# Kernel tuning notes

Measured on AMD Instinct MI355X. Metric: run time of the kernel, lower is better.

Reference implementation:

```python
import jax, jax.numpy as jnp
import numpy as np

EMBED = 1024
HEADS = 16
HEAD_DIM = EMBED // HEADS


def _rope(t):
    # t: (B, S, H, D) -> rotary embedding applied over last dim (GPT-NeoX rotate-half)
    B, S, H, D = t.shape
    half = D // 2
    inv_freq = 1.0 / (10000.0 ** (jnp.arange(0, half, dtype=jnp.float32) / half))
    freqs = jnp.arange(S, dtype=jnp.float32)[:, None] * inv_freq[None, :]  # (S, half)
    cos = jnp.cos(freqs)[None, :, None, :]
    sin = jnp.sin(freqs)[None, :, None, :]
    t1, t2 = t[..., :half], t[..., half:]
    return jnp.concatenate([t1 * cos - t2 * sin, t2 * cos + t1 * sin], axis=-1)


def setup_inputs() -> dict:
    key = jax.random.key(0)
    k1, k2, k3 = jax.random.split(key, 3)
    B, S = 2, 2048
    x = jax.random.normal(k1, (B, S, EMBED), dtype=jnp.float32)
    attn_mask = jnp.ones((B, S), dtype=bool)
    w_qkv = jax.random.normal(k2, (EMBED, 3 * EMBED), dtype=jnp.float32) * (1.0 / np.sqrt(EMBED))
    w_out = jax.random.normal(k3, (EMBED, EMBED), dtype=jnp.float32) * (1.0 / np.sqrt(EMBED))
    return {"x": x, "attn_mask": attn_mask, "w_qkv": w_qkv, "w_out": w_out, "is_causal": 1}


def reference(x, attn_mask, w_qkv, w_out, is_causal):
    B, S, E = x.shape
    qkv = x @ w_qkv                                   # (B, S, 3E)
    q, k, v = jnp.split(qkv, 3, axis=-1)
    q = q.reshape(B, S, HEADS, HEAD_DIM)
    k = k.reshape(B, S, HEADS, HEAD_DIM)
    v = v.reshape(B, S, HEADS, HEAD_DIM)
    q = _rope(q)
    k = _rope(k)
    scale = 1.0 / np.sqrt(HEAD_DIM)
    scores = jnp.einsum('bqhd,bkhd->bhqk', q, k) * scale  # (B, H, S, S)
    neg = jnp.asarray(-1e30, dtype=scores.dtype)
    if is_causal:
        causal = jnp.tril(jnp.ones((S, S), dtype=bool))
        scores = jnp.where(causal[None, None], scores, neg)
    else:
        scores = jnp.where(attn_mask[:, None, None, :], scores, neg)
    attn = jax.nn.softmax(scores, axis=-1)
    y = jnp.einsum('bhqk,bkhd->bqhd', attn, v).reshape(B, S, E)
    return y @ w_out
```

## Files before the change

kernel.cpp:

```cpp
#include <hip/hip_runtime.h>
#include <hip/hip_bf16.h>
#include <stdint.h>

typedef float v4f __attribute__((ext_vector_type(4)));
typedef short v8s __attribute__((ext_vector_type(8)));

#define LOG2E 1.44269504088896f
#define QSCALE (0.125f * LOG2E)
#define SOFTMAX_OFF 16.0f

__device__ __forceinline__ unsigned short f2bf(float f) {
    unsigned int u = __float_as_uint(f);
    u += 0x7fffu + ((u >> 16) & 1u);
    return (unsigned short)(u >> 16);
}

#define LDS_FENCE() __builtin_amdgcn_fence(__ATOMIC_ACQ_REL, "workgroup")

__device__ __forceinline__ void gload_lds16(const unsigned short* g, unsigned short* s) {
    __builtin_amdgcn_global_load_lds(
        (const __attribute__((address_space(1))) unsigned int*)g,
        (__attribute__((address_space(3))) unsigned int*)s, 16, 0, 0);
}

__global__ void k_prep(const float* __restrict__ x,
                       const float* __restrict__ w_qkv,
                       const float* __restrict__ w_out,
                       unsigned short* __restrict__ xb,
                       unsigned short* __restrict__ wqkvT,
                       unsigned short* __restrict__ woutT,
                       float2* __restrict__ rope) {
    __shared__ unsigned short tile[64][65];
    int id = blockIdx.x, t = threadIdx.x;
    if (id < 1024) {
        int base = id * 256 + t;
#pragma unroll
        for (int k = 0; k < 4; ++k) {
            int i = base + k * 262144;
            float4 v = ((const float4*)x)[i];
            ushort4 o;
            o.x = f2bf(v.x); o.y = f2bf(v.y); o.z = f2bf(v.z); o.w = f2bf(v.w);
            ((ushort4*)xb)[i] = o;
        }
        return;
    }
    id -= 1024;
    if (id < 256) {
        int idx = id * 256 + t;
        int s = idx >> 5, d = idx & 31;
        float inv = __expf(-(float)d * 0.28782313662425572f);
        float sn, cs;
        sincosf((float)s * inv, &sn, &cs);
        rope[idx] = make_float2(cs, sn);
        return;
    }
    id -= 256;
    const float* src; unsigned short* dst; int N, kb, nb;
    if (id < 768) { src = w_qkv; dst = wqkvT; N = 3072; nb = (id % 48) * 64; kb = (id / 48) * 64; }
    else { id -= 768; src = w_out; dst = woutT; N = 1024; nb = (id % 16) * 64; kb = (id / 16) * 64; }
    const int K = 1024;
    for (int i = 0; i < 16; ++i) {
        int e = t + i * 256;
        int n_l = e & 63, k_l = e >> 6;
        tile[n_l][k_l] = f2bf(src[(size_t)(kb + k_l) * N + nb + n_l]);
    }
    __syncthreads();
    for (int i = 0; i < 16; ++i) {
        int e = t + i * 256;
        int k_l = e & 63, n_l = e >> 6;
        dst[(size_t)(nb + n_l) * K + kb + k_l] = tile[n_l][k_l];
    }
}

__global__ __launch_bounds__(256) void k_gemm_qkv(
    const unsigned short* __restrict__ A,
    const unsigned short* __restrict__ Bt,
    const float2* __restrict__ rope,
    unsigned short* __restrict__ Qg,
    unsigned short* __restrict__ Kg,
    unsigned short* __restrict__ Vt) {
    const int K = 1024;
    __shared__ __align__(16) union {
        struct { unsigned short Ab[2][4096], Bb[2][4096]; } g;
        unsigned short vt[2][64][136];
    } sm;
    const int t = threadIdx.x;
    const int w = t >> 6, l = t & 63, quad = l >> 4, ln = l & 15;
    const int wm = (w >> 1) * 64, wn = (w & 1) * 64;
    const int mb = blockIdx.y * 128, nb = blockIdx.x * 128;

    v4f acc[4][4];
#pragma unroll
    for (int i = 0; i < 4; ++i)
#pragma unroll
        for (int j = 0; j < 4; ++j) acc[i][j] = (v4f){0.f, 0.f, 0.f, 0.f};

    auto stage = [&](int buf, int k0) {
#pragma unroll
        for (int u = 0; u < 2; ++u) {
            int e = t + u * 256;
            gload_lds16(A + (size_t)(mb + (e >> 2)) * K + k0 + (e & 3) * 8,
                        &sm.g.Ab[buf][(w * 64 + u * 256) * 8]);
            gload_lds16(Bt + (size_t)(nb + (e >> 2)) * K + k0 + (e & 3) * 8,
                        &sm.g.Bb[buf][(w * 64 + u * 256) * 8]);
        }
    };

    stage(0, 0);
    int buf = 0;
    for (int itk = 0; itk < 32; ++itk) {
        __syncthreads();
        if (itk + 1 < 32) stage(buf ^ 1, (itk + 1) * 32);
        v8s af[4], bfr[4];
#pragma unroll
        for (int i = 0; i < 4; ++i)
            af[i] = *(const v8s*)&sm.g.Ab[buf][(wm + i * 16 + ln) * 32 + quad * 8];
#pragma unroll
        for (int j = 0; j < 4; ++j)
            bfr[j] = *(const v8s*)&sm.g.Bb[buf][(wn + j * 16 + ln) * 32 + quad * 8];
#pragma unroll
        for (int i = 0; i < 4; ++i)
#pragma unroll
            for (int j = 0; j < 4; ++j)
                acc[i][j] = __builtin_amdgcn_mfma_f32_16x16x32_bf16(
                    af[i], bfr[j], acc[i][j], 0, 0, 0);
        buf ^= 1;
    }

    if (nb >= 2048) {
        __syncthreads();
        const int hh = wn >> 6;
#pragma unroll
        for (int i = 0; i < 4; ++i)
#pragma unroll
            for (int j = 0; j < 4; ++j) {
                int d = j * 16 + ln;
#pragma unroll
                for (int r = 0; r < 4; ++r)
                    sm.vt[hh][d][wm + i * 16 + quad * 4 + r] = f2bf(acc[i][j][r]);
            }
        __syncthreads();
        const int hbase = (nb & 1023) >> 6;
        const int b = mb >> 11, sbase = mb & 2047;
#pragma unroll
        for (int i = 0; i < 8; ++i) {
            int c = t + i * 256;
            int h2 = c >> 10, dd = (c >> 4) & 63, off = (c & 15) * 8;
            v8s val = *(const v8s*)&sm.vt[h2][dd][off];
            *(v8s*)(Vt + ((size_t)((b * 16 + hbase + h2) * 64 + dd) * 2048 + sbase + off)) = val;
        }
        return;
    }

    const int region = (nb + wn) >> 10;
    const int h = ((nb + wn) & 1023) >> 6;
    unsigned short* dst = region == 0 ? Qg : Kg;
    const float scale = region == 0 ? QSCALE : 1.0f;
#pragma unroll
    for (int jj = 0; jj < 2; ++jj) {
        const float2* rp = rope + jj * 16 + ln;
#pragma unroll
        for (int i = 0; i < 4; ++i)
#pragma unroll
            for (int r = 0; r < 4; ++r) {
                int row = mb + wm + i * 16 + quad * 4 + r;
                int s = row & 2047, b = row >> 11;
                float2 cs = rp[s * 32];
                float t1 = acc[i][jj][r], t2 = acc[i][jj + 2][r];
                size_t base = ((size_t)(b * 16 + h) * 2048 + s) * 64;
                dst[base + jj * 16 + ln]      = f2bf((t1 * cs.x - t2 * cs.y) * scale);
                dst[base + jj * 16 + ln + 32] = f2bf((t2 * cs.x + t1 * cs.y) * scale);
            }
    }
}

__global__ __launch_bounds__(256) void k_gemm_out(
    const unsigned short* __restrict__ A,
    const unsigned short* __restrict__ Bt,
    float* __restrict__ C) {
    const int K = 1024, N = 1024;
    __shared__ __align__(16) unsigned short Ab[2][4096];
    __shared__ __align__(16) unsigned short Bb[2][4096];
    const int t = threadIdx.x;
    const int w = t >> 6, l = t & 63, quad = l >> 4, ln = l & 15;
    const int wm = (w >> 1) * 64, wn = (w & 1) * 64;
    const int mb = blockIdx.y * 128, nb = blockIdx.x * 128;

    v4f acc[4][4];
#pragma unroll
    for (int i = 0; i < 4; ++i)
#pragma unroll
        for (int j = 0; j < 4; ++j) acc[i][j] = (v4f){0.f, 0.f, 0.f, 0.f};

    auto stage = [&](int buf, int k0) {
#pragma unroll
        for (int u = 0; u < 2; ++u) {
            int e = t + u * 256;
            gload_lds16(A + (size_t)(mb + (e >> 2)) * K + k0 + (e & 3) * 8,
                        &Ab[buf][(w * 64 + u * 256) * 8]);
            gload_lds16(Bt + (size_t)(nb + (e >> 2)) * K + k0 + (e & 3) * 8,
                        &Bb[buf][(w * 64 + u * 256) * 8]);
        }
    };

    stage(0, 0);
    int buf = 0;
    for (int itk = 0; itk < 32; ++itk) {
        __syncthreads();
        if (itk + 1 < 32) stage(buf ^ 1, (itk + 1) * 32);
        v8s af[4], bfr[4];
#pragma unroll
        for (int i = 0; i < 4; ++i)
            af[i] = *(const v8s*)&Ab[buf][(wm + i * 16 + ln) * 32 + quad * 8];
#pragma unroll
        for (int j = 0; j < 4; ++j)
            bfr[j] = *(const v8s*)&Bb[buf][(wn + j * 16 + ln) * 32 + quad * 8];
#pragma unroll
        for (int i = 0; i < 4; ++i)
#pragma unroll
            for (int j = 0; j < 4; ++j)
                acc[i][j] = __builtin_amdgcn_mfma_f32_16x16x32_bf16(
                    af[i], bfr[j], acc[i][j], 0, 0, 0);
        buf ^= 1;
    }

#pragma unroll
    for (int i = 0; i < 4; ++i) {
        int r0 = mb + wm + i * 16 + quad * 4;
#pragma unroll
        for (int j = 0; j < 4; ++j) {
            int c0 = nb + wn + j * 16 + ln;
#pragma unroll
            for (int r = 0; r < 4; ++r)
                C[(size_t)(r0 + r) * N + c0] = acc[i][j][r];
        }
    }
}

__global__ __launch_bounds__(256) void k_flash(
    const unsigned short* __restrict__ Qg,
    const unsigned short* __restrict__ Kg,
    const unsigned short* __restrict__ Vt,
    unsigned short* __restrict__ Og) {
    __shared__ __align__(16) unsigned short Kb[2][64 * 64];
    __shared__ __align__(16) unsigned short Vb[2][64 * 64];
    __shared__ __align__(16) unsigned short P[4][16][72];

    const int id = blockIdx.x;
    const int xcd = id & 7, slot = id >> 3;
    const int bh = xcd * 4 + (slot & 3);
    const int qt = 31 - (slot >> 2);
    const int qbase = qt * 64;
    const int nit = qt + 1;

    const int t = threadIdx.x, w = t >> 6, l = t & 63, quad = l >> 4, ln = l & 15;
    const int b = bh >> 4, h = bh & 15;

    const unsigned short* Qp = Qg + (size_t)bh * 2048 * 64;
    const unsigned short* Kp = Kg + (size_t)bh * 2048 * 64;
    const unsigned short* Vp = Vt + (size_t)bh * 64 * 2048;

    unsigned kst[2], vst[2];
    int cchunk = l & 7, rloc = l >> 3;
#pragma unroll
    for (int j = 0; j < 2; ++j) {
        int c = w + j * 4;
        int rr = c * 8 + rloc;
        int g = (cchunk + rr) & 7;
        kst[j] = (unsigned)(rr * 64 + g * 8);
        vst[j] = (unsigned)(rr * 2048 + g * 8);
    }
    const int c0 = ((quad - ln) & 7) * 8;
    const int c1 = ((quad + 4 - ln) & 7) * 8;
    const v8s ones = {0x3F80, 0x3F80, 0x3F80, 0x3F80, 0x3F80, 0x3F80, 0x3F80, 0x3F80};

    const int qrow = qbase + w * 16 + ln;
    v8s qf0 = *(const v8s*)(Qp + (size_t)qrow * 64 + quad * 8);
    v8s qf1 = *(const v8s*)(Qp + (size_t)qrow * 64 + quad * 8 + 32);

    v4f oacc[5];
#pragma unroll
    for (int dt = 0; dt < 5; ++dt) oacc[dt] = (v4f){0.f, 0.f, 0.f, 0.f};

    auto stage = [&](int buf, int kvb) {
        const unsigned short* kg = Kp + (size_t)kvb * 64;
        const unsigned short* vg = Vp + kvb;
#pragma unroll
        for (int j = 0; j < 2; ++j) {
            int c = w + j * 4;
            gload_lds16(kg + kst[j], &Kb[buf][c * 512]);
            gload_lds16(vg + vst[j], &Vb[buf][c * 512]);
        }
    };

    auto compute = [&](int buf, int it) {
        v4f sc[4];
#pragma unroll
        for (int kt = 0; kt < 4; ++kt) {
            int row = kt * 16 + ln;
            v8s k0 = *(const v8s*)&Kb[buf][row * 64 + c0];
            v8s k1 = *(const v8s*)&Kb[buf][row * 64 + c1];
            sc[kt] = (v4f){0.f, 0.f, 0.f, 0.f};
            sc[kt] = __builtin_amdgcn_mfma_f32_16x16x32_bf16(qf0, k0, sc[kt], 0, 0, 0);
            sc[kt] = __builtin_amdgcn_mfma_f32_16x16x32_bf16(qf1, k1, sc[kt], 0, 0, 0);
        }
        if (it == qt) {
            int q0 = qbase + w * 16 + quad * 4;
#pragma unroll
            for (int kt = 0; kt < 4; ++kt) {
                int kv = qbase + kt * 16 + ln;
#pragma unroll
                for (int r = 0; r < 4; ++r)
                    if (kv > q0 + r) sc[kt][r] = -1e30f;
            }
        }
#pragma unroll
        for (int kt = 0; kt < 4; ++kt)
#pragma unroll
            for (int r = 0; r < 4; ++r)
                sc[kt][r] = exp2f(sc[kt][r] - SOFTMAX_OFF);

#pragma unroll
        for (int kt = 0; kt < 4; ++kt) {
            union { __hip_bfloat162 hh; unsigned int u; } p01, p23;
            p01.hh = __float22bfloat162_rn(make_float2(sc[kt][0], sc[kt][1]));
            p23.hh = __float22bfloat162_rn(make_float2(sc[kt][2], sc[kt][3]));
            P[w][quad * 4 + 0][kt * 16 + ln] = (unsigned short)p01.u;
            P[w][quad * 4 + 1][kt * 16 + ln] = (unsigned short)(p01.u >> 16);
            P[w][quad * 4 + 2][kt * 16 + ln] = (unsigned short)p23.u;
            P[w][quad * 4 + 3][kt * 16 + ln] = (unsigned short)(p23.u >> 16);
        }
        LDS_FENCE();
        v8s pf0 = *(const v8s*)&P[w][ln][quad * 8];
        v8s pf1 = *(const v8s*)&P[w][ln][quad * 8 + 32];
        LDS_FENCE();
#pragma unroll
        for (int dt = 0; dt < 4; ++dt) {
            int row = dt * 16 + ln;
            v8s v0 = *(const v8s*)&Vb[buf][row * 64 + c0];
            v8s v1 = *(const v8s*)&Vb[buf][row * 64 + c1];
            oacc[dt] = __builtin_amdgcn_mfma_f32_16x16x32_bf16(pf0, v0, oacc[dt], 0, 0, 0);
            oacc[dt] = __builtin_amdgcn_mfma_f32_16x16x32_bf16(pf1, v1, oacc[dt], 0, 0, 0);
        }
        oacc[4] = __builtin_amdgcn_mfma_f32_16x16x32_bf16(pf0, ones, oacc[4], 0, 0, 0);
        oacc[4] = __builtin_amdgcn_mfma_f32_16x16x32_bf16(pf1, ones, oacc[4], 0, 0, 0);
    };

    stage(0, 0);
    int it = 0;
    for (;;) {
        __syncthreads();
        stage(1, (it + 1) * 64);
        compute(0, it);
        if (++it >= nit) break;
        __syncthreads();
        stage(0, (it + 1) * 64);
        compute(1, it);
        if (++it >= nit) break;
    }

    float rden[4];
#pragma unroll
    for (int r = 0; r < 4; ++r) rden[r] = 1.f / oacc[4][r];
#pragma unroll
    for (int dt = 0; dt < 4; ++dt)
#pragma unroll
        for (int r = 0; r < 4; ++r) {
            int s = qbase + w * 16 + quad * 4 + r;
            Og[(size_t)(b * 2048 + s) * 1024 + h * 64 + dt * 16 + ln] =
                f2bf(oacc[dt][r] * rden[r]);
        }
}

extern "C" void kernel_launch(void* const* d_in, const int* in_sizes, int n_in,
                              void* d_out, int out_size, void* d_ws, size_t ws_size,
                              hipStream_t stream) {
    const float* x     = (const float*)d_in[0];
    const float* w_qkv = (const float*)d_in[2];
    const float* w_out = (const float*)d_in[3];
    char* ws = (char*)d_ws;

    unsigned short* xb    = (unsigned short*)(ws);
    unsigned short* wqkvT = (unsigned short*)(ws + (size_t)(8 << 20));
    unsigned short* woutT = (unsigned short*)(ws + (size_t)(14 << 20));
    unsigned short* Qg    = (unsigned short*)(ws + (size_t)(16 << 20));
    unsigned short* Kg    = (unsigned short*)(ws + (size_t)(24 << 20));
    unsigned short* Vt    = (unsigned short*)(ws + (size_t)(32 << 20));
    unsigned short* Og    = (unsigned short*)(ws + (size_t)(40 << 20));
    float2*         rope  = (float2*)(ws + (size_t)(48 << 20));

    k_prep<<<2304, 256, 0, stream>>>(x, w_qkv, w_out, xb, wqkvT, woutT, rope);
    k_gemm_qkv<<<dim3(24, 32), 256, 0, stream>>>(xb, wqkvT, rope, Qg, Kg, Vt);
    k_flash<<<1024, 256, 0, stream>>>(Qg, Kg, Vt, Og);
    k_gemm_out<<<dim3(8, 32), 256, 0, stream>>>(Og, woutT, (float*)d_out);
}
```

Baseline: 195.2 us.

## Triple-buffer GEMM K-loop with partial vmcnt waits instead of full syncthreads

Both GEMM kernels move from double to triple LDS buffering and prefetch two K-tiles ahead. The barrier now waits only until the oldest stage's four global-to-LDS loads have landed (vmcnt(4)) rather than draining every outstanding load, so one tile stays in flight during compute. This is meant to hide global load latency behind the MFMA work, at the cost of 50% more LDS per block, which may lower occupancy. It also depends on the compiler's vmcnt accounting matching the inline waitcnt.

```diff
diff --git a/kernel.cpp b/kernel.cpp
--- a/kernel.cpp
+++ b/kernel.cpp
@@ -22,6 +22,19 @@
         (const __attribute__((address_space(1))) unsigned int*)g,
         (__attribute__((address_space(3))) unsigned int*)s, 16, 0, 0);
 }
+
+#define PIPE_BARRIER_KEEP4()                                   \
+    do {                                                       \
+        asm volatile("s_waitcnt vmcnt(4)" ::: "memory");       \
+        __builtin_amdgcn_s_barrier();                          \
+        asm volatile("" ::: "memory");                         \
+    } while (0)
+#define PIPE_BARRIER_DRAIN()                                   \
+    do {                                                       \
+        asm volatile("s_waitcnt vmcnt(0)" ::: "memory");       \
+        __builtin_amdgcn_s_barrier();                          \
+        asm volatile("" ::: "memory");                         \
+    } while (0)
 
 __global__ void k_prep(const float* __restrict__ x,
                        const float* __restrict__ w_qkv,
@@ -81,7 +94,7 @@
     unsigned short* __restrict__ Vt) {
     const int K = 1024;
     __shared__ __align__(16) union {
-        struct { unsigned short Ab[2][4096], Bb[2][4096]; } g;
+        struct { unsigned short Ab[3][4096], Bb[3][4096]; } g;
         unsigned short vt[2][64][136];
     } sm;
     const int t = threadIdx.x;
@@ -107,24 +120,29 @@
     };
 
     stage(0, 0);
-    int buf = 0;
+    stage(1, 32);
+    int cur = 0, nxt = 2;
     for (int itk = 0; itk < 32; ++itk) {
-        __syncthreads();
-        if (itk + 1 < 32) stage(buf ^ 1, (itk + 1) * 32);
+        if (itk < 31) PIPE_BARRIER_KEEP4();
+        else          PIPE_BARRIER_DRAIN();
+        if (itk + 2 < 32) {
+            stage(nxt, (itk + 2) * 32);
+            nxt = nxt == 2 ? 0 : nxt + 1;
+        }
         v8s af[4], bfr[4];
 #pragma unroll
         for (int i = 0; i < 4; ++i)
-            af[i] = *(const v8s*)&sm.g.Ab[buf][(wm + i * 16 + ln) * 32 + quad * 8];
+            af[i] = *(const v8s*)&sm.g.Ab[cur][(wm + i * 16 + ln) * 32 + quad * 8];
 #pragma unroll
         for (int j = 0; j < 4; ++j)
-            bfr[j] = *(const v8s*)&sm.g.Bb[buf][(wn + j * 16 + ln) * 32 + quad * 8];
+            bfr[j] = *(const v8s*)&sm.g.Bb[cur][(wn + j * 16 + ln) * 32 + quad * 8];
 #pragma unroll
         for (int i = 0; i < 4; ++i)
 #pragma unroll
             for (int j = 0; j < 4; ++j)
                 acc[i][j] = __builtin_amdgcn_mfma_f32_16x16x32_bf16(
                     af[i], bfr[j], acc[i][j], 0, 0, 0);
-        buf ^= 1;
+        cur = cur == 2 ? 0 : cur + 1;
     }
 
     if (nb >= 2048) {
@@ -179,8 +197,8 @@
     const unsigned short* __restrict__ Bt,
     float* __restrict__ C) {
     const int K = 1024, N = 1024;
-    __shared__ __align__(16) unsigned short Ab[2][4096];
-    __shared__ __align__(16) unsigned short Bb[2][4096];
+    __shared__ __align__(16) unsigned short Ab[3][4096];
+    __shared__ __align__(16) unsigned short Bb[3][4096];
     const int t = threadIdx.x;
     const int w = t >> 6, l = t & 63, quad = l >> 4, ln = l & 15;
     const int wm = (w >> 1) * 64, wn = (w & 1) * 64;
@@ -204,24 +222,29 @@
     };
 
     stage(0, 0);
-    int buf = 0;
+    stage(1, 32);
+    int cur = 0, nxt = 2;
     for (int itk = 0; itk < 32; ++itk) {
-        __syncthreads();
-        if (itk + 1 < 32) stage(buf ^ 1, (itk + 1) * 32);
+        if (itk < 31) PIPE_BARRIER_KEEP4();
+        else          PIPE_BARRIER_DRAIN();
+        if (itk + 2 < 32) {
+            stage(nxt, (itk + 2) * 32);
+            nxt = nxt == 2 ? 0 : nxt + 1;
+        }
         v8s af[4], bfr[4];
 #pragma unroll
         for (int i = 0; i < 4; ++i)
-            af[i] = *(const v8s*)&Ab[buf][(wm + i * 16 + ln) * 32 + quad * 8];
+            af[i] = *(const v8s*)&Ab[cur][(wm + i * 16 + ln) * 32 + quad * 8];
 #pragma unroll
         for (int j = 0; j < 4; ++j)
-            bfr[j] = *(const v8s*)&Bb[buf][(wn + j * 16 + ln) * 32 + quad * 8];
+            bfr[j] = *(const v8s*)&Bb[cur][(wn + j * 16 + ln) * 32 + quad * 8];
 #pragma unroll
         for (int i = 0; i < 4; ++i)
 #pragma unroll
             for (int j = 0; j < 4; ++j)
                 acc[i][j] = __builtin_amdgcn_mfma_f32_16x16x32_bf16(
                     af[i], bfr[j], acc[i][j], 0, 0, 0);
-        buf ^= 1;
+        cur = cur == 2 ? 0 : cur + 1;
     }
 
 #pragma unroll
```

After: 193.3 us. About the same (-1.0%).
